# Kernel tuning notes

Measured on AMD Instinct MI355X. Metric: run time of the kernel, lower is better.

## Reference

```python
import jax, jax.numpy as jnp
import numpy as np

B, T, IN, N, D, H, R, C = 1024, 50, 784, 128, 40, 200, 4, 5
GAMMA = 0.95  # usage decay (standard LRUA)


def setup_inputs() -> dict:
    key = jax.random.key(0)
    ks = jax.random.split(key, 9)
    xdim = IN + C + R * D  # controller input: [x, offset_label, read_vectors]

    def u(k, shape, s=0.1):
        return jax.random.uniform(k, shape, jnp.float32, -s, s)

    return {
        "images": jax.random.normal(ks[0], (B, T, IN), jnp.float32),
        "labels": jax.random.randint(ks[1], (B, T), 0, C),
        "Wx": u(ks[2], (xdim, 4 * H)),
        "Wh": u(ks[3], (H, 4 * H)),
        "b_lstm": u(ks[4], (4 * H,)),
        "Wp": u(ks[5], (H, R * (D + 1))),
        "bp": u(ks[6], (R * (D + 1),)),
        "Wc": u(ks[7], (H + R * D, C)),
        "bc": u(ks[8], (C,)),
    }


def _forward(images, labels_oh, Wx, Wh, b_lstm, Wp, bp, Wc, bc):
    # offset targets: labels shifted right by one timestep, zeros at t=0
    offset = jnp.concatenate([jnp.zeros_like(labels_oh[:, :1]), labels_oh[:, :-1]], axis=1)
    inp = jnp.concatenate([images, offset], axis=2)  # [B, T, IN+C]

    M0 = jnp.full((B, N, D), 1e-6, jnp.float32)
    r0 = jnp.full((B, R * D), 1e-6, jnp.float32)
    h0 = jnp.zeros((B, H), jnp.float32)
    c0 = jnp.zeros((B, H), jnp.float32)
    wu0 = jax.nn.one_hot(jnp.zeros((B,), jnp.int32), N)
    wr0 = jnp.tile(jax.nn.one_hot(jnp.zeros((B,), jnp.int32), N)[:, None, :], (1, R, 1))

    def step(carry, x_t):
        M, r, h, c, wu, wr = carry
        # LSTM controller
        ctrl_in = jnp.concatenate([x_t, r], axis=-1)
        gates = ctrl_in @ Wx + h @ Wh + b_lstm
        i, f, g, o = jnp.split(gates, 4, axis=-1)
        c_new = jax.nn.sigmoid(f) * c + jax.nn.sigmoid(i) * jnp.tanh(g)
        h_new = jax.nn.sigmoid(o) * jnp.tanh(c_new)
        # per-head key + interpolation gate
        p = (h_new @ Wp + bp).reshape(B, R, D + 1)
        k = jnp.tanh(p[..., :D])            # [B, R, D]
        sigma = jax.nn.sigmoid(p[..., D:])  # [B, R, 1]
        # least-used addressing from previous usage weights
        _, lu_idx = jax.lax.top_k(-wu, R)                   # R least-used slots
        w_lu = jax.nn.one_hot(lu_idx, N).sum(axis=1)        # [B, N]
        # cosine-similarity content addressing -> read weights
        kn = k / (jnp.linalg.norm(k, axis=-1, keepdims=True) + 1e-8)
        Mn = M / (jnp.linalg.norm(M, axis=-1, keepdims=True) + 1e-8)
        w_r = jax.nn.softmax(jnp.einsum('brd,bnd->brn', kn, Mn), axis=-1)  # [B,R,N]
        # write weights: interpolate prev read and least-used
        w_w = sigma * wr + (1.0 - sigma) * w_lu[:, None, :]
        wu_new = GAMMA * wu + w_r.sum(axis=1) + w_w.sum(axis=1)
        # erase least-used slot, then additive write of keys
        M_erased = M * (1.0 - jax.nn.one_hot(lu_idx[:, -1], N))[:, :, None]
        M_new = M_erased + jnp.einsum('brn,brd->bnd', w_w, k)
        # read from updated memory
        r_new = jnp.einsum('brn,bnd->brd', w_r, M_new).reshape(B, R * D)
        out = jnp.concatenate([h_new, r_new], axis=-1)
        logits = out @ Wc + bc
        return (M_new, r_new, h_new, c_new, wu_new, w_r), logits

    _, logits = jax.lax.scan(step, (M0, r0, h0, c0, wu0, wr0), jnp.swapaxes(inp, 0, 1))
    return jnp.swapaxes(logits, 0, 1)  # [B, T, C]


def reference(images, labels, Wx, Wh, b_lstm, Wp, bp, Wc, bc):
    labels_oh = jax.nn.one_hot(labels, C, dtype=jnp.float32)  # [B,T,C]
    logits = _forward(images, labels_oh, Wx, Wh, b_lstm, Wp, bp, Wc, bc)
    probs = jax.nn.softmax(logits, axis=2)
    pred = jnp.argmax(probs, axis=2).reshape(-1)
    out = probs.reshape(-1, C)
    # faithful to original: CrossEntropyLoss applied to already-softmaxed probs with soft targets
    loss = jnp.mean(-jnp.sum(labels_oh.reshape(-1, C) * jax.nn.log_softmax(out, axis=-1), axis=-1))
    tgt = labels.reshape(-1)
    acc = jnp.mean((pred == tgt).astype(jnp.float32))
    return out, loss, acc
```

## Files before the change

kernel.cpp:

```cpp
#include <hip/hip_runtime.h>
#include <hip/hip_bf16.h>
#include <math.h>

#define B_  1024
#define T_  50
#define IN_ 784
#define N_  128
#define D_  40
#define H_  200
#define R_  4
#define C_  5
#define GAMMA_ 0.95f
#define G4H_ 800
#define PDIM_ 164
#define RD_ 160
#define OUTF_ 360
#define MSZ_ 5120
#define MST_ 42
#define KP_ 800
#define GSTR_ 1024

#define AKB_ 24
#define BKB_ 36
#define WXP_N 643072
#define W2P_N (BKB_ * GSTR_ * 32)
#define APK_N (AKB_ * B_ * 32)

typedef __bf16 bf16x8 __attribute__((ext_vector_type(8)));
typedef __bf16 bf16x4 __attribute__((ext_vector_type(4)));
typedef float  fx4    __attribute__((ext_vector_type(4)));

__device__ __forceinline__ float sigmoidf_(float x) { return 1.f / (1.f + expf(-x)); }

__device__ __forceinline__ void load_lds16(const void* g, void* l) {
    __builtin_amdgcn_global_load_lds(
        (const __attribute__((address_space(1))) unsigned int*)g,
        (__attribute__((address_space(3))) unsigned int*)l, 16, 0, 0);
}

__global__ __launch_bounds__(256) void pack_kernel(
    const float* __restrict__ Wx, const float* __restrict__ Wh,
    const float* __restrict__ Wp,
    __bf16* __restrict__ WxP, __bf16* __restrict__ W2P)
{
    int idx = blockIdx.x * 256 + threadIdx.x;
    if (idx < WXP_N) {
        int kb = idx / 25600, rem = idx - kb * 25600;
        int n = rem >> 5, q8 = rem & 31;
        int k = kb * 32 + q8;
        WxP[idx] = (k < IN_ && kb < 25) ? (__bf16)Wx[(size_t)k * G4H_ + n] : (__bf16)0.0f;
    }
    if (idx < W2P_N) {
        int kb = idx >> 15;
        int rem = idx & 32767;
        int n = rem >> 5, q8 = rem & 31;
        int kl = (kb < 12 ? kb : (kb < 24 ? kb - 12 : kb - 24)) * 32 + q8;
        __bf16 o = (__bf16)0.0f;
        float v = 0.f; bool has = false;
        if (n < G4H_) {
            if (kl < OUTF_) {
                v = (kl < H_) ? Wh[(size_t)kl * G4H_ + n]
                              : Wx[(size_t)(789 + kl - H_) * G4H_ + n];
                has = true;
            }
        } else if (n < G4H_ + PDIM_) {
            if (kl < H_) { v = Wp[(size_t)kl * PDIM_ + (n - G4H_)]; has = true; }
        }
        if (has) {
            __bf16 hi = (__bf16)v;
            o = (kb < 24) ? hi : (__bf16)(v - (float)hi);
        }
        W2P[idx] = o;
    }
}

__global__ void init_kernel(float* Cst, float* Mg, float* wug, float* wrg,
                            __bf16* Apack, float* scal)
{
    size_t i = (size_t)blockIdx.x * blockDim.x + threadIdx.x;
    size_t stride = (size_t)gridDim.x * blockDim.x;
    for (size_t j = i; j < (size_t)B_ * MSZ_; j += stride) Mg[j] = 1e-6f;
    for (size_t j = i; j < (size_t)B_ * H_; j += stride) Cst[j] = 0.f;
    for (size_t j = i; j < (size_t)B_ * N_; j += stride) wug[j] = ((j & (N_ - 1)) == 0) ? 1.f : 0.f;
    for (size_t j = i; j < (size_t)B_ * R_ * N_; j += stride) wrg[j] = ((j & (N_ - 1)) == 0) ? 1.f : 0.f;
    for (size_t j = i; j < (size_t)APK_N; j += stride) {
        int kb = (int)(j >> 15);
        int q8 = (int)(j & 31);
        int kl = (kb % 12) * 32 + q8;
        float v = (kl >= H_ && kl < OUTF_) ? 1e-6f : 0.f;
        __bf16 hi = (__bf16)v;
        Apack[j] = (kb < 12) ? hi : (__bf16)(v - (float)hi);
    }
    if (i < 2) scal[i] = 0.f;
}

__global__ __launch_bounds__(256) void img_convert(
    const float* __restrict__ images, __bf16* __restrict__ img)
{
    long long gi = (long long)blockIdx.x * 256 + threadIdx.x;
    if (gi * 4 >= (long long)T_ * B_ * KP_) return;
    long long m = (gi * 4) / KP_;
    int k = (int)((gi * 4) - m * KP_);
    int t = (int)(m >> 10), b = (int)(m & (B_ - 1));
    bf16x4 o;
    if (k < IN_) {
        const float4 v = *(const float4*)&images[((size_t)b * T_ + t) * IN_ + k];
        o[0] = (__bf16)v.x; o[1] = (__bf16)v.y; o[2] = (__bf16)v.z; o[3] = (__bf16)v.w;
    } else {
        o[0] = o[1] = o[2] = o[3] = (__bf16)0.0f;
    }
    *(bf16x4*)&img[(size_t)m * KP_ + k] = o;
}

__global__ __launch_bounds__(256) void gx_mfma(
    const __bf16* __restrict__ img, const __bf16* __restrict__ WxP,
    const int* __restrict__ labels, const float* __restrict__ Wx,
    const float* __restrict__ b_lstm, float* __restrict__ Gx)
{
    __shared__ __bf16 A_lds[2048];
    __shared__ __bf16 B_lds[5120];

    const int tid  = threadIdx.x;
    const int lane = tid & 63, w = tid >> 6;
    const int quad = lane >> 4, ln = lane & 15;
    const int swzl = (ln & 3) ^ ((ln >> 2) & 3);
    const int row0 = blockIdx.x * 64;
    const int n0   = blockIdx.y * 160;
    const int rw   = (w >> 1) * 32;
    const int cw   = (w & 1) * 80;

    fx4 acc[2][5];
    #pragma unroll
    for (int i = 0; i < 2; i++)
        #pragma unroll
        for (int j = 0; j < 5; j++) acc[i][j] = (fx4)0.0f;

    for (int kb = 0; kb < 25; kb++) {
        {
            int m = tid >> 2, c = tid & 3;
            int q = c ^ ((m & 3) ^ ((m >> 2) & 3));
            load_lds16(img + (size_t)(row0 + m) * KP_ + kb * 32 + q * 8,
                       &A_lds[(size_t)(w * 64) * 8]);
        }
        #pragma unroll
        for (int p = 0; p < 3; p++) {
            if (p * 4 + w < 10) {
                int cc = p * 256 + tid;
                int n = cc >> 2, c = cc & 3;
                int q = c ^ ((n & 3) ^ ((n >> 2) & 3));
                load_lds16(WxP + ((size_t)kb * G4H_ + n0 + n) * 32 + q * 8,
                           &B_lds[(size_t)(p * 256 + w * 64) * 8]);
            }
        }
        __syncthreads();

        bf16x8 a[2], bb[5];
        #pragma unroll
        for (int mi = 0; mi < 2; mi++)
            a[mi] = *(const bf16x8*)&A_lds[((rw + mi * 16 + ln) * 4 + (quad ^ swzl)) * 8];
        #pragma unroll
        for (int ni = 0; ni < 5; ni++)
            bb[ni] = *(const bf16x8*)&B_lds[((cw + ni * 16 + ln) * 4 + (quad ^ swzl)) * 8];
        #pragma unroll
        for (int mi = 0; mi < 2; mi++)
            #pragma unroll
            for (int ni = 0; ni < 5; ni++)
                acc[mi][ni] = __builtin_amdgcn_mfma_f32_16x16x32_bf16(a[mi], bb[ni], acc[mi][ni], 0, 0, 0);
        __syncthreads();
    }

    #pragma unroll
    for (int mi = 0; mi < 2; mi++) {
        #pragma unroll
        for (int rr = 0; rr < 4; rr++) {
            int row = row0 + rw + mi * 16 + quad * 4 + rr;
            int t = row >> 10, b = row & (B_ - 1);
            int lbl = (t > 0) ? labels[b * T_ + t - 1] : -1;
            #pragma unroll
            for (int ni = 0; ni < 5; ni++) {
                int col = n0 + cw + ni * 16 + ln;
                float add = b_lstm[col];
                if (lbl >= 0) add += Wx[(size_t)(IN_ + lbl) * G4H_ + col];
                Gx[(size_t)row * G4H_ + col] = acc[mi][ni][rr] + add;
            }
        }
    }
}

__global__ __launch_bounds__(256) void rec_mfma(
    const __bf16* __restrict__ Apack, const __bf16* __restrict__ W2P,
    const float* __restrict__ Gxt, const float* __restrict__ bp,
    float* __restrict__ gates)
{
    __shared__ __bf16 A_lds[6144];
    __shared__ __bf16 B_lds[6144];

    const int tid  = threadIdx.x;
    const int lane = tid & 63, w = tid >> 6;
    const int quad = lane >> 4, ln = lane & 15;
    const int swzl = (ln & 3) ^ ((ln >> 2) & 3);
    const int row0 = blockIdx.x * 32;
    const int col0 = blockIdx.y * 32;
    const int mw   = (w >> 1) * 16;
    const int nw   = (w & 1) * 16;

    fx4 acc = (fx4)0.0f;

    for (int it = 0; it < 6; it++) {
        #pragma unroll
        for (int p = 0; p < 3; p++) {
            int cc = p * 256 + tid;
            int kbl = cc >> 7, row = (cc >> 2) & 31, c = cc & 3;
            int q = c ^ ((row & 3) ^ ((row >> 2) & 3));
            int kbg = it * 6 + kbl;
            int kba = (kbg < AKB_) ? kbg : kbg - AKB_;
            load_lds16(Apack + ((size_t)kba * B_ + row0 + row) * 32 + q * 8,
                       &A_lds[(size_t)(p * 256 + w * 64) * 8]);
        }
        #pragma unroll
        for (int p = 0; p < 3; p++) {
            int cc = p * 256 + tid;
            int kbl = cc >> 7, n = (cc >> 2) & 31, c = cc & 3;
            int q = c ^ ((n & 3) ^ ((n >> 2) & 3));
            int kbg = it * 6 + kbl;
            load_lds16(W2P + ((size_t)kbg * GSTR_ + col0 + n) * 32 + q * 8,
                       &B_lds[(size_t)(p * 256 + w * 64) * 8]);
        }
        __syncthreads();

        #pragma unroll
        for (int s = 0; s < 6; s++) {
            bf16x8 a0 = *(const bf16x8*)&A_lds[((s * 32 + mw + ln) * 4 + (quad ^ swzl)) * 8];
            bf16x8 b0 = *(const bf16x8*)&B_lds[((s * 32 + nw + ln) * 4 + (quad ^ swzl)) * 8];
            acc = __builtin_amdgcn_mfma_f32_16x16x32_bf16(a0, b0, acc, 0, 0, 0);
        }
        __syncthreads();
    }

    #pragma unroll
    for (int rr = 0; rr < 4; rr++) {
        int row = row0 + mw + quad * 4 + rr;
        int col = col0 + nw + ln;
        float add;
        if (col < G4H_)              add = Gxt[(size_t)row * G4H_ + col];
        else if (col < G4H_ + PDIM_) add = bp[col - G4H_];
        else                         add = 0.f;
        gates[(size_t)row * GSTR_ + col] = acc[rr] + add;
    }
}

__global__ __launch_bounds__(256) void step_kernel(
    const float* __restrict__ gates, __bf16* __restrict__ Apack, float* __restrict__ Cst,
    float* __restrict__ Mg, float* __restrict__ wug, float* __restrict__ wrg,
    const float* __restrict__ Wc, const float* __restrict__ bc,
    float* __restrict__ out, int t)
{
    const int b = blockIdx.x;
    const int tid = threadIdx.x;
    const int lane = tid & 63, w = tid >> 6;
    const int nn = tid >> 1, dh = tid & 1, d0 = dh * 20;

    __shared__ float M_s[N_ * MST_];
    __shared__ float h_s[H_];
    __shared__ float k_s[RD_];
    __shared__ float sig_s[R_];
    __shared__ float wu_s[N_];
    __shared__ int   lu_s[R_];
    __shared__ float wrn_s[R_ * N_];
    __shared__ float ww_s[R_ * N_];
    __shared__ float rn_s[RD_];
    __shared__ float red[160];

    float m[20];

    if (tid < H_) {
        const float gi = gates[(size_t)b * GSTR_ + tid];
        const float gf = gates[(size_t)b * GSTR_ + H_ + tid];
        const float gg = gates[(size_t)b * GSTR_ + 2 * H_ + tid];
        const float go = gates[(size_t)b * GSTR_ + 3 * H_ + tid];
        const float c_old = Cst[b * H_ + tid];
        const float cn = sigmoidf_(gf) * c_old + sigmoidf_(gi) * tanhf(gg);
        const float hn = sigmoidf_(go) * tanhf(cn);
        Cst[b * H_ + tid] = cn;
        h_s[tid] = hn;
        __bf16 hi = (__bf16)hn;
        __bf16 lo = (__bf16)(hn - (float)hi);
        const int kb = tid >> 5, q8 = tid & 31;
        Apack[((size_t)kb * B_ + b) * 32 + q8] = hi;
        Apack[((size_t)(kb + 12) * B_ + b) * 32 + q8] = lo;
    }
    if (tid < N_) wu_s[tid] = wug[b * N_ + tid];
    {
        const float* src = Mg + (size_t)b * MSZ_ + nn * D_ + d0;
        #pragma unroll
        for (int j = 0; j < 20; j += 4) {
            float4 v = *(const float4*)&src[j];
            m[j] = v.x; m[j + 1] = v.y; m[j + 2] = v.z; m[j + 3] = v.w;
        }
    }
    __syncthreads();

    if (tid < PDIM_) {
        float acc = gates[(size_t)b * GSTR_ + G4H_ + tid];
        int r = tid / (D_ + 1), d = tid - r * (D_ + 1);
        if (d < D_) k_s[r * D_ + d] = tanhf(acc);
        else        sig_s[r] = sigmoidf_(acc);
    }
    if (w == 3) {
        float v0 = wu_s[lane], v1 = wu_s[lane + 64];
        #pragma unroll
        for (int r4 = 0; r4 < R_; r4++) {
            float v; int idx;
            if (v1 < v0) { v = v1; idx = lane + 64; } else { v = v0; idx = lane; }
            #pragma unroll
            for (int off = 32; off > 0; off >>= 1) {
                float ov = __shfl_down(v, off);
                int   oi = __shfl_down(idx, off);
                if (ov < v || (ov == v && oi < idx)) { v = ov; idx = oi; }
            }
            int bi = __shfl(idx, 0);
            if (lane == 0) lu_s[r4] = bi;
            if (lane == bi) v0 = 3.0e38f;
            if (lane + 64 == bi) v1 = 3.0e38f;
        }
    }
    __syncthreads();

    {
        float nr = 0.f;
        #pragma unroll
        for (int j = 0; j < 20; j++) nr += m[j] * m[j];
        float dt[4];
        #pragma unroll
        for (int r = 0; r < 4; r++) {
            float s = 0.f;
            const float* kr = &k_s[r * D_ + d0];
            #pragma unroll
            for (int j = 0; j < 20; j += 4) {
                float4 kv = *(const float4*)&kr[j];
                s += m[j] * kv.x + m[j + 1] * kv.y + m[j + 2] * kv.z + m[j + 3] * kv.w;
            }
            dt[r] = s;
        }
        nr += __shfl_xor(nr, 1);
        #pragma unroll
        for (int r = 0; r < 4; r++) dt[r] += __shfl_xor(dt[r], 1);
        const float den = sqrtf(nr) + 1e-8f;
        if (dh == 0) { wrn_s[nn] = dt[0] / den;          wrn_s[N_ + nn] = dt[1] / den; }
        else         { wrn_s[2 * N_ + nn] = dt[2] / den; wrn_s[3 * N_ + nn] = dt[3] / den; }
    }
    __syncthreads();

    {
        const int r = w;
        float kv = (lane < D_) ? k_s[r * D_ + lane] * k_s[r * D_ + lane] : 0.f;
        #pragma unroll
        for (int off = 32; off > 0; off >>= 1) kv += __shfl_xor(kv, off);
        const float kinv = 1.f / (sqrtf(kv) + 1e-8f);

        const int n0i = lane, n1i = lane + 64;
        float s0 = wrn_s[r * N_ + n0i] * kinv;
        float s1 = wrn_s[r * N_ + n1i] * kinv;
        const float sg = sig_s[r];
        float wlu0 = (n0i == lu_s[0] || n0i == lu_s[1] || n0i == lu_s[2] || n0i == lu_s[3]) ? 1.f : 0.f;
        float wlu1 = (n1i == lu_s[0] || n1i == lu_s[1] || n1i == lu_s[2] || n1i == lu_s[3]) ? 1.f : 0.f;
        ww_s[r * N_ + n0i] = sg * wrg[(size_t)b * (R_ * N_) + r * N_ + n0i] + (1.f - sg) * wlu0;
        ww_s[r * N_ + n1i] = sg * wrg[(size_t)b * (R_ * N_) + r * N_ + n1i] + (1.f - sg) * wlu1;
        float mx = fmaxf(s0, s1);
        #pragma unroll
        for (int off = 32; off > 0; off >>= 1) mx = fmaxf(mx, __shfl_xor(mx, off));
        float e0 = expf(s0 - mx), e1 = expf(s1 - mx);
        float sm = e0 + e1;
        #pragma unroll
        for (int off = 32; off > 0; off >>= 1) sm += __shfl_xor(sm, off);
        const float inv = 1.f / sm;
        e0 *= inv; e1 *= inv;
        wrn_s[r * N_ + n0i] = e0;
        wrn_s[r * N_ + n1i] = e1;
        wrg[(size_t)b * (R_ * N_) + r * N_ + n0i] = e0;
        wrg[(size_t)b * (R_ * N_) + r * N_ + n1i] = e1;
    }
    __syncthreads();

    if (tid < N_) {
        float acc = GAMMA_ * wu_s[tid];
        #pragma unroll
        for (int r = 0; r < R_; r++) acc += wrn_s[r * N_ + tid] + ww_s[r * N_ + tid];
        wug[b * N_ + tid] = acc;
    }
    {
        const int lu4 = lu_s[3];
        if (nn == lu4) {
            #pragma unroll
            for (int j = 0; j < 20; j++) m[j] = 0.f;
        }
        float wgt[4];
        #pragma unroll
        for (int r = 0; r < 4; r++) wgt[r] = ww_s[r * N_ + nn];
        #pragma unroll
        for (int r = 0; r < 4; r++) {
            const float* kr = &k_s[r * D_ + d0];
            const float g = wgt[r];
            #pragma unroll
            for (int j = 0; j < 20; j += 4) {
                float4 kv = *(const float4*)&kr[j];
                m[j]     += g * kv.x;
                m[j + 1] += g * kv.y;
                m[j + 2] += g * kv.z;
                m[j + 3] += g * kv.w;
            }
        }
        float* mrow = &M_s[nn * MST_ + d0];
        float* gdst = Mg + (size_t)b * MSZ_ + nn * D_ + d0;
        #pragma unroll
        for (int j = 0; j < 20; j += 4) {
            *(float2*)&mrow[j]     = make_float2(m[j], m[j + 1]);
            *(float2*)&mrow[j + 2] = make_float2(m[j + 2], m[j + 3]);
            *(float4*)&gdst[j]     = make_float4(m[j], m[j + 1], m[j + 2], m[j + 3]);
        }
    }
    __syncthreads();

    if (tid < RD_) {
        const int r = tid / D_, d = tid - r * D_;
        const float* wrow = &wrn_s[r * N_];
        float a0 = 0.f, a1 = 0.f, a2 = 0.f, a3 = 0.f;
        #pragma unroll 8
        for (int n2 = 0; n2 < N_; n2 += 4) {
            float4 wv = *(const float4*)&wrow[n2];
            a0 += wv.x * M_s[(n2 + 0) * MST_ + d];
            a1 += wv.y * M_s[(n2 + 1) * MST_ + d];
            a2 += wv.z * M_s[(n2 + 2) * MST_ + d];
            a3 += wv.w * M_s[(n2 + 3) * MST_ + d];
        }
        const float acc = (a0 + a1) + (a2 + a3);
        rn_s[tid] = acc;
        __bf16 hi = (__bf16)acc;
        __bf16 lo = (__bf16)(acc - (float)hi);
        const int kp = H_ + tid;
        const int kb = kp >> 5, q8 = kp & 31;
        Apack[((size_t)kb * B_ + b) * 32 + q8] = hi;
        Apack[((size_t)(kb + 12) * B_ + b) * 32 + q8] = lo;
    }
    __syncthreads();

    if (tid < 160) {
        int c = tid >> 5, seg = tid & 31;
        float acc = 0.f;
        for (int j = seg; j < OUTF_; j += 32) {
            float v = (j < H_) ? h_s[j] : rn_s[j - H_];
            acc += v * Wc[j * C_ + c];
        }
        red[tid] = acc;
    }
    __syncthreads();

    if (w == 0) {
        float lg = 0.f;
        if (lane < C_) {
            lg = bc[lane];
            #pragma unroll
            for (int s = 0; s < 32; s++) lg += red[lane * 32 + s];
        }
        float l0 = __shfl(lg, 0), l1 = __shfl(lg, 1), l2 = __shfl(lg, 2);
        float l3 = __shfl(lg, 3), l4 = __shfl(lg, 4);
        if (lane == 0) {
            float mx = fmaxf(fmaxf(fmaxf(l0, l1), fmaxf(l2, l3)), l4);
            float e0 = expf(l0 - mx), e1 = expf(l1 - mx), e2 = expf(l2 - mx);
            float e3 = expf(l3 - mx), e4 = expf(l4 - mx);
            float inv = 1.f / (e0 + e1 + e2 + e3 + e4);
            float* o = out + ((size_t)b * T_ + t) * C_;
            o[0] = e0 * inv; o[1] = e1 * inv; o[2] = e2 * inv; o[3] = e3 * inv; o[4] = e4 * inv;
        }
    }
}

__global__ __launch_bounds__(256) void loss_kernel(
    const float* __restrict__ out, const int* __restrict__ labels, float* __restrict__ la)
{
    int row = blockIdx.x * 256 + threadIdx.x;
    float li = 0.f, ai = 0.f;
    if (row < B_ * T_) {
        float p[C_];
        #pragma unroll
        for (int c = 0; c < C_; c++) p[c] = out[(size_t)row * C_ + c];
        int tgt = labels[row];
        float mx = p[0];
        #pragma unroll
        for (int c = 1; c < C_; c++) mx = fmaxf(mx, p[c]);
        float sm = 0.f;
        #pragma unroll
        for (int c = 0; c < C_; c++) sm += expf(p[c] - mx);
        li = (mx + logf(sm) - p[tgt]) * (1.f / (B_ * T_));
        int pred = 0; float bv = p[0];
        #pragma unroll
        for (int c = 1; c < C_; c++) if (p[c] > bv) { bv = p[c]; pred = c; }
        ai = (pred == tgt) ? (1.f / (B_ * T_)) : 0.f;
    }
    for (int off = 32; off > 0; off >>= 1) {
        li += __shfl_down(li, off);
        ai += __shfl_down(ai, off);
    }
    if ((threadIdx.x & 63) == 0) {
        atomicAdd(&la[0], li);
        atomicAdd(&la[1], ai);
    }
}

extern "C" void kernel_launch(void* const* d_in, const int* in_sizes, int n_in,
                              void* d_out, int out_size, void* d_ws, size_t ws_size,
                              hipStream_t stream)
{
    const float* images = (const float*)d_in[0];
    const int*   labels = (const int*)d_in[1];
    const float* Wx     = (const float*)d_in[2];
    const float* Wh     = (const float*)d_in[3];
    const float* b_lstm = (const float*)d_in[4];
    const float* Wp     = (const float*)d_in[5];
    const float* bp     = (const float*)d_in[6];
    const float* Wc     = (const float*)d_in[7];
    const float* bc     = (const float*)d_in[8];
    float* out = (float*)d_out;

    float* ws = (float*)d_ws;
    float* gates = ws;
    float* Cst   = gates + (size_t)B_ * GSTR_;
    float* Mg    = Cst   + (size_t)B_ * H_;
    float* wug   = Mg    + (size_t)B_ * MSZ_;
    float* wrg   = wug   + (size_t)B_ * N_;
    float* Gx    = wrg   + (size_t)B_ * R_ * N_;
    __bf16* imgb = (__bf16*)(Gx + (size_t)T_ * B_ * G4H_);
    __bf16* WxP  = imgb + (size_t)T_ * B_ * KP_;
    __bf16* W2P  = WxP  + (size_t)WXP_N;
    __bf16* Apack = W2P + (size_t)W2P_N;

    pack_kernel<<<(W2P_N + 255) / 256, 256, 0, stream>>>(Wx, Wh, Wp, WxP, W2P);
    init_kernel<<<1024, 256, 0, stream>>>(Cst, Mg, wug, wrg, Apack, out + (size_t)B_ * T_ * C_);

    img_convert<<<(int)(((long long)T_ * B_ * KP_ / 4 + 255) / 256), 256, 0, stream>>>(images, imgb);
    gx_mfma<<<dim3(T_ * B_ / 64, 5), 256, 0, stream>>>(imgb, WxP, labels, Wx, b_lstm, Gx);

    for (int t = 0; t < T_; t++) {
        rec_mfma<<<dim3(B_ / 32, GSTR_ / 32), 256, 0, stream>>>(
            Apack, W2P, Gx + (size_t)t * B_ * G4H_, bp, gates);
        step_kernel<<<B_, 256, 0, stream>>>(
            gates, Apack, Cst, Mg, wug, wrg, Wc, bc, out, t);
    }

    loss_kernel<<<(B_ * T_) / 256, 256, 0, stream>>>(out, labels, out + (size_t)B_ * T_ * C_);
}
```

Baseline: 1.884 ms.

## Double-buffer LDS tiles in input and recurrent MFMA GEMMs

Both the input-projection GEMM and the per-step recurrent GEMM now use two LDS buffers, prefetching the next K-block with direct-to-LDS loads while the current one is consumed by MFMAs. Explicit vmcnt waits and raw s_barrier calls, fenced by sched_barrier, replace the full __syncthreads. The recurrent kernel's K chunk shrinks from 6 to 4 blocks per iteration so the doubled buffers fit. The aim is to hide global-load latency behind the matrix ops. The hand-counted vmcnt values are fragile if the compiler emits a different number of loads per wave.

```diff
diff --git a/kernel.cpp b/kernel.cpp
--- a/kernel.cpp
+++ b/kernel.cpp
@@ -117,8 +117,8 @@
     const int* __restrict__ labels, const float* __restrict__ Wx,
     const float* __restrict__ b_lstm, float* __restrict__ Gx)
 {
-    __shared__ __bf16 A_lds[2048];
-    __shared__ __bf16 B_lds[5120];
+    __shared__ __bf16 A_lds[2][2048];
+    __shared__ __bf16 B_lds[2][5120];
 
     const int tid  = threadIdx.x;
     const int lane = tid & 63, w = tid >> 6;
@@ -135,38 +135,68 @@
         #pragma unroll
         for (int j = 0; j < 5; j++) acc[i][j] = (fx4)0.0f;
 
+    {
+        int m = tid >> 2, c = tid & 3;
+        int q = c ^ ((m & 3) ^ ((m >> 2) & 3));
+        load_lds16(img + (size_t)(row0 + m) * KP_ + q * 8,
+                   &A_lds[0][(size_t)(w * 64) * 8]);
+    }
+    #pragma unroll
+    for (int p = 0; p < 3; p++) {
+        if (p * 4 + w < 10) {
+            int cc = p * 256 + tid;
+            int n = cc >> 2, c = cc & 3;
+            int q = c ^ ((n & 3) ^ ((n >> 2) & 3));
+            load_lds16(WxP + ((size_t)0 * G4H_ + n0 + n) * 32 + q * 8,
+                       &B_lds[0][(size_t)(p * 256 + w * 64) * 8]);
+        }
+    }
+
     for (int kb = 0; kb < 25; kb++) {
-        {
-            int m = tid >> 2, c = tid & 3;
-            int q = c ^ ((m & 3) ^ ((m >> 2) & 3));
-            load_lds16(img + (size_t)(row0 + m) * KP_ + kb * 32 + q * 8,
-                       &A_lds[(size_t)(w * 64) * 8]);
-        }
-        #pragma unroll
-        for (int p = 0; p < 3; p++) {
-            if (p * 4 + w < 10) {
-                int cc = p * 256 + tid;
-                int n = cc >> 2, c = cc & 3;
-                int q = c ^ ((n & 3) ^ ((n >> 2) & 3));
-                load_lds16(WxP + ((size_t)kb * G4H_ + n0 + n) * 32 + q * 8,
-                           &B_lds[(size_t)(p * 256 + w * 64) * 8]);
-            }
-        }
-        __syncthreads();
+        const int cb = kb & 1, nb = cb ^ 1;
+        if (kb + 1 < 25) {
+            const int kn = kb + 1;
+            {
+                int m = tid >> 2, c = tid & 3;
+                int q = c ^ ((m & 3) ^ ((m >> 2) & 3));
+                load_lds16(img + (size_t)(row0 + m) * KP_ + kn * 32 + q * 8,
+                           &A_lds[nb][(size_t)(w * 64) * 8]);
+            }
+            #pragma unroll
+            for (int p = 0; p < 3; p++) {
+                if (p * 4 + w < 10) {
+                    int cc = p * 256 + tid;
+                    int n = cc >> 2, c = cc & 3;
+                    int q = c ^ ((n & 3) ^ ((n >> 2) & 3));
+                    load_lds16(WxP + ((size_t)kn * G4H_ + n0 + n) * 32 + q * 8,
+                               &B_lds[nb][(size_t)(p * 256 + w * 64) * 8]);
+                }
+            }
+            if (w < 2) asm volatile("s_waitcnt vmcnt(4)" ::: "memory");
+            else       asm volatile("s_waitcnt vmcnt(3)" ::: "memory");
+        } else {
+            asm volatile("s_waitcnt vmcnt(0)" ::: "memory");
+        }
+        __builtin_amdgcn_sched_barrier(0);
+        __builtin_amdgcn_s_barrier();
+        __builtin_amdgcn_sched_barrier(0);
 
         bf16x8 a[2], bb[5];
         #pragma unroll
         for (int mi = 0; mi < 2; mi++)
-            a[mi] = *(const bf16x8*)&A_lds[((rw + mi * 16 + ln) * 4 + (quad ^ swzl)) * 8];
+            a[mi] = *(const bf16x8*)&A_lds[cb][((rw + mi * 16 + ln) * 4 + (quad ^ swzl)) * 8];
         #pragma unroll
         for (int ni = 0; ni < 5; ni++)
-            bb[ni] = *(const bf16x8*)&B_lds[((cw + ni * 16 + ln) * 4 + (quad ^ swzl)) * 8];
+            bb[ni] = *(const bf16x8*)&B_lds[cb][((cw + ni * 16 + ln) * 4 + (quad ^ swzl)) * 8];
         #pragma unroll
         for (int mi = 0; mi < 2; mi++)
             #pragma unroll
             for (int ni = 0; ni < 5; ni++)
                 acc[mi][ni] = __builtin_amdgcn_mfma_f32_16x16x32_bf16(a[mi], bb[ni], acc[mi][ni], 0, 0, 0);
-        __syncthreads();
+
+        __builtin_amdgcn_sched_barrier(0);
+        __builtin_amdgcn_s_barrier();
+        __builtin_amdgcn_sched_barrier(0);
     }
 
     #pragma unroll
@@ -192,8 +222,8 @@
     const float* __restrict__ Gxt, const float* __restrict__ bp,
     float* __restrict__ gates)
 {
-    __shared__ __bf16 A_lds[6144];
-    __shared__ __bf16 B_lds[6144];
+    __shared__ __bf16 A_lds[2][4096];
+    __shared__ __bf16 B_lds[2][4096];
 
     const int tid  = threadIdx.x;
     const int lane = tid & 63, w = tid >> 6;
@@ -206,35 +236,64 @@
 
     fx4 acc = (fx4)0.0f;
 
-    for (int it = 0; it < 6; it++) {
-        #pragma unroll
-        for (int p = 0; p < 3; p++) {
-            int cc = p * 256 + tid;
-            int kbl = cc >> 7, row = (cc >> 2) & 31, c = cc & 3;
-            int q = c ^ ((row & 3) ^ ((row >> 2) & 3));
-            int kbg = it * 6 + kbl;
-            int kba = (kbg < AKB_) ? kbg : kbg - AKB_;
-            load_lds16(Apack + ((size_t)kba * B_ + row0 + row) * 32 + q * 8,
-                       &A_lds[(size_t)(p * 256 + w * 64) * 8]);
-        }
-        #pragma unroll
-        for (int p = 0; p < 3; p++) {
-            int cc = p * 256 + tid;
-            int kbl = cc >> 7, n = (cc >> 2) & 31, c = cc & 3;
-            int q = c ^ ((n & 3) ^ ((n >> 2) & 3));
-            int kbg = it * 6 + kbl;
-            load_lds16(W2P + ((size_t)kbg * GSTR_ + col0 + n) * 32 + q * 8,
-                       &B_lds[(size_t)(p * 256 + w * 64) * 8]);
-        }
-        __syncthreads();
-
-        #pragma unroll
-        for (int s = 0; s < 6; s++) {
-            bf16x8 a0 = *(const bf16x8*)&A_lds[((s * 32 + mw + ln) * 4 + (quad ^ swzl)) * 8];
-            bf16x8 b0 = *(const bf16x8*)&B_lds[((s * 32 + nw + ln) * 4 + (quad ^ swzl)) * 8];
+    #pragma unroll
+    for (int p = 0; p < 2; p++) {
+        int cc = p * 256 + tid;
+        int kbl = cc >> 7, row = (cc >> 2) & 31, c = cc & 3;
+        int q = c ^ ((row & 3) ^ ((row >> 2) & 3));
+        load_lds16(Apack + ((size_t)kbl * B_ + row0 + row) * 32 + q * 8,
+                   &A_lds[0][(size_t)(p * 256 + w * 64) * 8]);
+    }
+    #pragma unroll
+    for (int p = 0; p < 2; p++) {
+        int cc = p * 256 + tid;
+        int kbl = cc >> 7, n = (cc >> 2) & 31, c = cc & 3;
+        int q = c ^ ((n & 3) ^ ((n >> 2) & 3));
+        load_lds16(W2P + ((size_t)kbl * GSTR_ + col0 + n) * 32 + q * 8,
+                   &B_lds[0][(size_t)(p * 256 + w * 64) * 8]);
+    }
+
+    for (int it = 0; it < 9; it++) {
+        const int cb = it & 1, nb = cb ^ 1;
+        if (it + 1 < 9) {
+            const int in2 = it + 1;
+            #pragma unroll
+            for (int p = 0; p < 2; p++) {
+                int cc = p * 256 + tid;
+                int kbl = cc >> 7, row = (cc >> 2) & 31, c = cc & 3;
+                int q = c ^ ((row & 3) ^ ((row >> 2) & 3));
+                int kbg = in2 * 4 + kbl;
+                int kba = (kbg < AKB_) ? kbg : kbg - AKB_;
+                load_lds16(Apack + ((size_t)kba * B_ + row0 + row) * 32 + q * 8,
+                           &A_lds[nb][(size_t)(p * 256 + w * 64) * 8]);
+            }
+            #pragma unroll
+            for (int p = 0; p < 2; p++) {
+                int cc = p * 256 + tid;
+                int kbl = cc >> 7, n = (cc >> 2) & 31, c = cc & 3;
+                int q = c ^ ((n & 3) ^ ((n >> 2) & 3));
+                int kbg = in2 * 4 + kbl;
+                load_lds16(W2P + ((size_t)kbg * GSTR_ + col0 + n) * 32 + q * 8,
+                           &B_lds[nb][(size_t)(p * 256 + w * 64) * 8]);
+            }
+            asm volatile("s_waitcnt vmcnt(4)" ::: "memory");
+        } else {
+            asm volatile("s_waitcnt vmcnt(0)" ::: "memory");
+        }
+        __builtin_amdgcn_sched_barrier(0);
+        __builtin_amdgcn_s_barrier();
+        __builtin_amdgcn_sched_barrier(0);
+
+        #pragma unroll
+        for (int s = 0; s < 4; s++) {
+            bf16x8 a0 = *(const bf16x8*)&A_lds[cb][((s * 32 + mw + ln) * 4 + (quad ^ swzl)) * 8];
+            bf16x8 b0 = *(const bf16x8*)&B_lds[cb][((s * 32 + nw + ln) * 4 + (quad ^ swzl)) * 8];
             acc = __builtin_amdgcn_mfma_f32_16x16x32_bf16(a0, b0, acc, 0, 0, 0);
         }
-        __syncthreads();
+
+        __builtin_amdgcn_sched_barrier(0);
+        __builtin_amdgcn_s_barrier();
+        __builtin_amdgcn_sched_barrier(0);
     }
 
     #pragma unroll
```

New measurement: 1.879 ms. About the same (-0.2%).
